# Kernel optimization log

Measured on AMD Instinct MI355X. Metric: run time of the kernel, lower is better.

Reference implementation:

```python
import jax, jax.numpy as jnp
import numpy as np

N = 50000   # nodes
E = 800000  # edges (avg degree 16)
H = 128     # hidden_dim / emb_dim
OUT = 128   # out_dim
NUM_BOND_TYPE = 6
NUM_BOND_DIR = 6


def setup_inputs() -> dict:
    key = jax.random.key(0)
    ks = jax.random.split(key, 12)
    s = 0.05
    return {
        "x": jax.random.normal(ks[0], (N, H), jnp.float32),
        "edge_index": jax.random.randint(ks[1], (2, E), 0, N),
        "edge_attr": jax.random.randint(ks[2], (E, 2), 0, 6),
        "prelu_a": jnp.float32(0.25),  # PReLU single shared slope (torch default)
        "W_enc": jax.random.normal(ks[3], (H, H), jnp.float32) * s,  # enc_to_dec, no bias
        "edge_emb1": jax.random.normal(ks[4], (NUM_BOND_TYPE, H), jnp.float32) * s,
        "edge_emb2": jax.random.normal(ks[5], (NUM_BOND_DIR, H), jnp.float32) * s,
        "W1": jax.random.normal(ks[6], (H, 2 * H), jnp.float32) * s,
        "b1": jnp.zeros((2 * H,), jnp.float32),
        "W2": jax.random.normal(ks[7], (2 * H, OUT), jnp.float32) * s,
        "b2": jnp.zeros((OUT,), jnp.float32),
    }


def reference(x, edge_index, edge_attr, prelu_a, W_enc, edge_emb1, edge_emb2, W1, b1, W2, b2):
    n = x.shape[0]
    # GNNDecoder: PReLU then enc_to_dec linear (no bias)
    x = jnp.where(x > 0, x, prelu_a * x)
    x = x @ W_enc

    # GINConv.forward: add self loops, self-loop edge_attr = [5, 0]
    loop = jnp.arange(n)
    src = jnp.concatenate([edge_index[0], loop])  # [E+N]
    dst = jnp.concatenate([edge_index[1], loop])  # [E+N]
    ea1 = jnp.concatenate([edge_attr[:, 0], jnp.full((n,), 5, edge_attr.dtype)])
    ea2 = jnp.concatenate([edge_attr[:, 1], jnp.zeros((n,), edge_attr.dtype)])

    # edge embedding lookup + gather-add message + scatter-add aggregate
    edge_emb = edge_emb1[ea1] + edge_emb2[ea2]          # [E+N, H]
    msg = x[src] + edge_emb                             # message(x_j, edge_attr)
    agg = jax.ops.segment_sum(msg, dst, num_segments=n)  # aggr='add'

    # update: MLP Linear(H,2H) -> SiLU -> Linear(2H,OUT)
    h = jax.nn.silu(agg @ W1 + b1)
    return h @ W2 + b2
```

## Files before the change

### kernel.cpp

```cpp
#include <hip/hip_runtime.h>

typedef unsigned short u16;
typedef unsigned int   u32;
typedef __attribute__((ext_vector_type(8))) short short8;
typedef __attribute__((ext_vector_type(4))) float f32x4;

__device__ __forceinline__ float bl(u32 u){ union{u32 i; float f;} c; c.i = u << 16; return c.f; }
__device__ __forceinline__ float bh(u32 u){ union{u32 i; float f;} c; c.i = u & 0xffff0000u; return c.f; }
__device__ __forceinline__ u16 f2b(float f){
  union{float f; u32 i;} c; c.f = f;
  return (u16)((c.i + 0x8000u) >> 16);
}
__device__ __forceinline__ u32 pk2(float a, float b){
  union{float f; u32 i;} x, y; x.f = a; y.f = b;
  return ((x.i + 0x8000u) >> 16) | ((y.i + 0x8000u) & 0xffff0000u);
}
__device__ __forceinline__ void acc4(float* a, uint2 xq, uint2 eq){
  a[0] += bl(xq.x) + bl(eq.x);  a[1] += bh(xq.x) + bh(eq.x);
  a[2] += bl(xq.y) + bl(eq.y);  a[3] += bh(xq.y) + bh(eq.y);
}

__global__ __launch_bounds__(256) void k_setup(
    const float* __restrict__ Wenc, const float* __restrict__ W1,
    const float* __restrict__ W2, u16* __restrict__ WencT,
    u16* __restrict__ W1T, u16* __restrict__ W2T,
    int* __restrict__ cnt, int N)
{
  int i = blockIdx.x * 256 + threadIdx.x;
  if (i < 16384) {
    int n = i >> 7, k = i & 127;
    WencT[i] = f2b(Wenc[k * 128 + n]);
  } else if (i < 49152) {
    int j = i - 16384;
    int n = j >> 7, k = j & 127;
    W1T[j] = f2b(W1[k * 256 + n]);
  } else if (i < 81920) {
    int j = i - 49152;
    int n = j >> 8, k = j & 255;
    W2T[j] = f2b(W2[k * 128 + n]);
  } else {
    int j = i - 81920;
    if (j < N) cnt[j] = 0;
  }
}

__global__ __launch_bounds__(256) void k_enc_count(
    const float* __restrict__ x, const float* __restrict__ pa,
    const u16* __restrict__ WT, u16* __restrict__ xenc, int N,
    const int* __restrict__ ei, int* __restrict__ cnt,
    int* __restrict__ rank, int E, int encBlocks)
{
  if ((int)blockIdx.x >= encBlocks) {
    int e = ((int)blockIdx.x - encBlocks) * 256 + threadIdx.x;
    if (e < E) rank[e] = atomicAdd(&cnt[ei[E + e]], 1);
    return;
  }

  const int K = 128, SK = 136, NT = 8;
  __shared__ u16 sB[128 * SK];

  const int t = threadIdx.x;
  #pragma unroll
  for (int j = 0; j < 8; j++) {
    int i = t + 256 * j;
    int n = i >> 4, k8 = i & 15;
    *(uint4*)&sB[n * SK + k8 * 8] = *(const uint4*)&WT[n * K + k8 * 8];
  }
  __syncthreads();

  const float slope = pa[0];
  const int lane = t & 63, wave = t >> 6, quad = lane >> 4, l16 = lane & 15;
  const int m0 = blockIdx.x * 128 + wave * 32;
  if (m0 >= N) return;

  f32x4 acc[2][NT];
  #pragma unroll
  for (int mr = 0; mr < 2; mr++)
    #pragma unroll
    for (int nt = 0; nt < NT; nt++) acc[mr][nt] = (f32x4){0.f, 0.f, 0.f, 0.f};

  #pragma unroll
  for (int ks = 0; ks < 4; ks++) {
    const int k0 = ks * 32 + quad * 8;
    union { u32 u[4]; short8 s; } a[2];
    #pragma unroll
    for (int mr = 0; mr < 2; mr++) {
      int row = m0 + mr * 16 + l16; row = min(row, N - 1);
      const float4* ap = (const float4*)&x[(size_t)row * 128 + k0];
      float4 f0 = ap[0], f1 = ap[1];
      float v0 = f0.x > 0.f ? f0.x : slope * f0.x;
      float v1 = f0.y > 0.f ? f0.y : slope * f0.y;
      float v2 = f0.z > 0.f ? f0.z : slope * f0.z;
      float v3 = f0.w > 0.f ? f0.w : slope * f0.w;
      float v4 = f1.x > 0.f ? f1.x : slope * f1.x;
      float v5 = f1.y > 0.f ? f1.y : slope * f1.y;
      float v6 = f1.z > 0.f ? f1.z : slope * f1.z;
      float v7 = f1.w > 0.f ? f1.w : slope * f1.w;
      a[mr].u[0] = pk2(v0, v1); a[mr].u[1] = pk2(v2, v3);
      a[mr].u[2] = pk2(v4, v5); a[mr].u[3] = pk2(v6, v7);
    }
    #pragma unroll
    for (int nt = 0; nt < NT; nt++) {
      short8 b = *(const short8*)&sB[(nt * 16 + l16) * SK + k0];
      acc[0][nt] = __builtin_amdgcn_mfma_f32_16x16x32_bf16(a[0].s, b, acc[0][nt], 0, 0, 0);
      acc[1][nt] = __builtin_amdgcn_mfma_f32_16x16x32_bf16(a[1].s, b, acc[1][nt], 0, 0, 0);
    }
  }

  #pragma unroll
  for (int mr = 0; mr < 2; mr++)
    #pragma unroll
    for (int nt = 0; nt < NT; nt++) {
      int col = nt * 16 + l16;
      #pragma unroll
      for (int r = 0; r < 4; r++) {
        int row = m0 + mr * 16 + quad * 4 + r;
        if (row < N) xenc[(size_t)row * 128 + col] = f2b(acc[mr][nt][r]);
      }
    }
}

__global__ __launch_bounds__(256) void k_scan_block(
    const int* __restrict__ cnt, int* __restrict__ offs,
    int* __restrict__ bsum, int n)
{
  __shared__ int sS[256];
  const int b = blockIdx.x, t = threadIdx.x;
  const int i0 = b * 1024 + t * 4;
  int4 v = make_int4(0, 0, 0, 0);
  if (i0 + 3 < n) v = *(const int4*)&cnt[i0];
  else {
    if (i0     < n) v.x = cnt[i0];
    if (i0 + 1 < n) v.y = cnt[i0 + 1];
    if (i0 + 2 < n) v.z = cnt[i0 + 2];
  }
  int s = v.x + v.y + v.z + v.w;
  sS[t] = s;
  __syncthreads();
  for (int d = 1; d < 256; d <<= 1) {
    int val = (t >= d) ? sS[t - d] : 0;
    __syncthreads();
    sS[t] += val;
    __syncthreads();
  }
  int ex = sS[t] - s;
  if (t == 255) bsum[b] = sS[t];
  int o0 = ex, o1 = o0 + v.x, o2 = o1 + v.y, o3 = o2 + v.z;
  if (i0     < n) offs[i0]     = o0;
  if (i0 + 1 < n) offs[i0 + 1] = o1;
  if (i0 + 2 < n) offs[i0 + 2] = o2;
  if (i0 + 3 < n) offs[i0 + 3] = o3;
}

__global__ __launch_bounds__(256) void k_scan_add(
    int* __restrict__ offs, const int* __restrict__ bsum,
    int nb, int n, int E)
{
  __shared__ int sOff;
  const int t = threadIdx.x;
  const int i = blockIdx.x * 256 + t;
  const int myb = (blockIdx.x * 256) >> 10;
  if (t == 0) {
    int s = 0;
    for (int j = 0; j < myb; j++) s += bsum[j];
    sOff = s;
  }
  __syncthreads();
  if (i < n) offs[i] += sOff;
  if (i == n) offs[n] = E;
}

__global__ __launch_bounds__(256) void k_fill(
    const int* __restrict__ ei, const int* __restrict__ ea,
    const int* __restrict__ offs, const int* __restrict__ rank,
    u32* __restrict__ recs, int E)
{
  int e = blockIdx.x * 256 + threadIdx.x;
  if (e >= E) return;
  int src = ei[e];
  int dst = ei[E + e];
  int2 a = *(const int2*)&ea[2 * e];
  int pos = offs[dst] + rank[e];
  recs[pos] = (u32)src | ((u32)(a.x * 6 + a.y) << 26);
}

__global__ __launch_bounds__(256) void k_gather(
    const int* __restrict__ offs, const u32* __restrict__ recs,
    const float* __restrict__ e1, const float* __restrict__ e2,
    const u32* __restrict__ xenc32, u32* __restrict__ aggb, int N)
{
  __shared__ u32 sE[36 * 64];

  const int t = threadIdx.x;
  for (int i = t; i < 36 * 64; i += 256) {
    int comb = i >> 6, l = i & 63;
    int c1 = comb / 6, c2 = comb - c1 * 6;
    float2 v1 = *(const float2*)&e1[c1 * 128 + 2 * l];
    float2 v2 = *(const float2*)&e2[c2 * 128 + 2 * l];
    sE[i] = pk2(v1.x + v2.x, v1.y + v2.y);
  }
  __syncthreads();

  const int v = blockIdx.x * 4 + (t >> 6);
  if (v >= N) return;
  const int lane = t & 63, g = lane >> 5, sub = lane & 31;
  const u32 M = 0x3ffffffu;

  float a[4];
  #pragma unroll
  for (int j = 0; j < 4; j++) a[j] = 0.f;

  if (g == 0) {
    uint2 xq = *(const uint2*)&xenc32[(size_t)v * 64 + sub * 2];
    uint2 eq = *(const uint2*)&sE[30 * 64 + sub * 2];
    acc4(a, xq, eq);
  }

  const int beg = offs[v], end = offs[v + 1];
  for (int base = beg; base < end; base += 64) {
    u32 rv = 0;
    if (base + lane < end) rv = recs[base + lane];
    const int cnt = min(64, end - base);
    const int npair = cnt >> 1;
    int jj = 0;
    for (; jj + 4 <= npair; jj += 4) {
      u32 r0 = __shfl(rv, (jj + 0) * 2 + g);
      u32 r1 = __shfl(rv, (jj + 1) * 2 + g);
      u32 r2 = __shfl(rv, (jj + 2) * 2 + g);
      u32 r3 = __shfl(rv, (jj + 3) * 2 + g);
      uint2 x0 = *(const uint2*)&xenc32[(size_t)(r0 & M) * 64 + sub * 2];
      uint2 x1 = *(const uint2*)&xenc32[(size_t)(r1 & M) * 64 + sub * 2];
      uint2 x2 = *(const uint2*)&xenc32[(size_t)(r2 & M) * 64 + sub * 2];
      uint2 x3 = *(const uint2*)&xenc32[(size_t)(r3 & M) * 64 + sub * 2];
      uint2 e0 = *(const uint2*)&sE[(r0 >> 26) * 64 + sub * 2];
      uint2 e1q = *(const uint2*)&sE[(r1 >> 26) * 64 + sub * 2];
      uint2 e2q = *(const uint2*)&sE[(r2 >> 26) * 64 + sub * 2];
      uint2 e3q = *(const uint2*)&sE[(r3 >> 26) * 64 + sub * 2];
      acc4(a, x0, e0); acc4(a, x1, e1q); acc4(a, x2, e2q); acc4(a, x3, e3q);
    }
    for (; jj < npair; jj++) {
      u32 r = __shfl(rv, jj * 2 + g);
      uint2 xq = *(const uint2*)&xenc32[(size_t)(r & M) * 64 + sub * 2];
      uint2 eq = *(const uint2*)&sE[(r >> 26) * 64 + sub * 2];
      acc4(a, xq, eq);
    }
    if (cnt & 1) {
      u32 r = __shfl(rv, cnt - 1);
      if (g == 0) {
        uint2 xq = *(const uint2*)&xenc32[(size_t)(r & M) * 64 + sub * 2];
        uint2 eq = *(const uint2*)&sE[(r >> 26) * 64 + sub * 2];
        acc4(a, xq, eq);
      }
    }
  }

  #pragma unroll
  for (int j = 0; j < 4; j++) a[j] += __shfl_xor(a[j], 32);

  if (g == 0) {
    uint2 o;
    o.x = pk2(a[0], a[1]);
    o.y = pk2(a[2], a[3]);
    *(uint2*)&aggb[(size_t)v * 64 + sub * 2] = o;
  }
}

__global__ __launch_bounds__(256) void k_mlp(
    const u16* __restrict__ aggb, const u16* __restrict__ W1T,
    const float* __restrict__ b1, const u16* __restrict__ W2T,
    const float* __restrict__ b2, float* __restrict__ out, int N)
{
  const int SK = 136;
  __shared__ u16 sW[128 * SK];
  __shared__ u16 sH[128 * SK];
  __shared__ float sB1[256];
  __shared__ float sB2[128];

  const int t = threadIdx.x;
  const int lane = t & 63, wave = t >> 6, quad = lane >> 4, l16 = lane & 15;
  const int m0 = blockIdx.x * 128 + wave * 32;

  if (t < 128) sB2[t] = b2[t];
  sB1[t] = b1[t];

  union { uint4 q; short8 s; } a[2][4];
  #pragma unroll
  for (int mr = 0; mr < 2; mr++) {
    int row = min(m0 + mr * 16 + l16, N - 1);
    #pragma unroll
    for (int ks = 0; ks < 4; ks++)
      a[mr][ks].q = *(const uint4*)&aggb[(size_t)row * 128 + ks * 32 + quad * 8];
  }

  f32x4 acc2[2][8];
  #pragma unroll
  for (int mr = 0; mr < 2; mr++)
    #pragma unroll
    for (int nt = 0; nt < 8; nt++) acc2[mr][nt] = (f32x4){0.f, 0.f, 0.f, 0.f};

  for (int half = 0; half < 2; half++) {
    #pragma unroll
    for (int j = 0; j < 8; j++) {
      int i = t + 256 * j;
      int n = i >> 4, k8 = i & 15;
      *(uint4*)&sW[n * SK + k8 * 8] =
          *(const uint4*)&W1T[(size_t)(half * 128 + n) * 128 + k8 * 8];
    }
    __syncthreads();

    f32x4 acc1[2][8];
    #pragma unroll
    for (int mr = 0; mr < 2; mr++)
      #pragma unroll
      for (int nt = 0; nt < 8; nt++) acc1[mr][nt] = (f32x4){0.f, 0.f, 0.f, 0.f};

    #pragma unroll
    for (int ks = 0; ks < 4; ks++) {
      const int k0 = ks * 32 + quad * 8;
      #pragma unroll
      for (int nt = 0; nt < 8; nt++) {
        short8 b = *(const short8*)&sW[(nt * 16 + l16) * SK + k0];
        acc1[0][nt] = __builtin_amdgcn_mfma_f32_16x16x32_bf16(a[0][ks].s, b, acc1[0][nt], 0, 0, 0);
        acc1[1][nt] = __builtin_amdgcn_mfma_f32_16x16x32_bf16(a[1][ks].s, b, acc1[1][nt], 0, 0, 0);
      }
    }

    #pragma unroll
    for (int mr = 0; mr < 2; mr++)
      #pragma unroll
      for (int nt = 0; nt < 8; nt++) {
        int col = nt * 16 + l16;
        float bias = sB1[half * 128 + col];
        #pragma unroll
        for (int r = 0; r < 4; r++) {
          float z = acc1[mr][nt][r] + bias;
          float s = z / (1.f + __expf(-z));
          sH[(wave * 32 + mr * 16 + quad * 4 + r) * SK + col] = f2b(s);
        }
      }
    __syncthreads();

    #pragma unroll
    for (int j = 0; j < 8; j++) {
      int i = t + 256 * j;
      int n = i >> 4, k8 = i & 15;
      *(uint4*)&sW[n * SK + k8 * 8] =
          *(const uint4*)&W2T[(size_t)n * 256 + half * 128 + k8 * 8];
    }
    __syncthreads();

    #pragma unroll
    for (int ks = 0; ks < 4; ks++) {
      const int k0 = ks * 32 + quad * 8;
      union { uint4 q; short8 s; } ah[2];
      #pragma unroll
      for (int mr = 0; mr < 2; mr++)
        ah[mr].q = *(const uint4*)&sH[(wave * 32 + mr * 16 + l16) * SK + k0];
      #pragma unroll
      for (int nt = 0; nt < 8; nt++) {
        short8 b = *(const short8*)&sW[(nt * 16 + l16) * SK + k0];
        acc2[0][nt] = __builtin_amdgcn_mfma_f32_16x16x32_bf16(ah[0].s, b, acc2[0][nt], 0, 0, 0);
        acc2[1][nt] = __builtin_amdgcn_mfma_f32_16x16x32_bf16(ah[1].s, b, acc2[1][nt], 0, 0, 0);
      }
    }
    __syncthreads();
  }

  #pragma unroll
  for (int mr = 0; mr < 2; mr++)
    #pragma unroll
    for (int nt = 0; nt < 8; nt++) {
      int col = nt * 16 + l16;
      float bias = sB2[col];
      #pragma unroll
      for (int r = 0; r < 4; r++) {
        int row = m0 + mr * 16 + quad * 4 + r;
        if (row < N) out[(size_t)row * 128 + col] = acc2[mr][nt][r] + bias;
      }
    }
}

extern "C" void kernel_launch(void* const* d_in, const int* in_sizes, int n_in,
                              void* d_out, int out_size, void* d_ws, size_t ws_size,
                              hipStream_t stream) {
  const float* x    = (const float*)d_in[0];
  const int*   ei   = (const int*)d_in[1];
  const int*   ea   = (const int*)d_in[2];
  const float* pa   = (const float*)d_in[3];
  const float* Wenc = (const float*)d_in[4];
  const float* e1   = (const float*)d_in[5];
  const float* e2   = (const float*)d_in[6];
  const float* W1   = (const float*)d_in[7];
  const float* b1   = (const float*)d_in[8];
  const float* W2   = (const float*)d_in[9];
  const float* b2   = (const float*)d_in[10];
  float* out = (float*)d_out;

  const int N = in_sizes[0] / 128;
  const int E = in_sizes[1] / 2;

  char* ws = (char*)d_ws;
  size_t off = 0;
  auto alloc = [&](size_t bytes) {
    void* p = ws + off;
    off = (off + bytes + 255) & ~(size_t)255;
    return p;
  };
  u16*   xenc   = (u16*)  alloc((size_t)N * 128 * 2);
  u32*   aggb   = (u32*)  alloc((size_t)N * 64 * 4);
  int*   cnt    = (int*)  alloc((size_t)N * 4);
  int*   offs   = (int*)  alloc((size_t)(N + 1) * 4);
  int*   rank   = (int*)  alloc((size_t)E * 4);
  int*   bsum   = (int*)  alloc(256 * 4);
  u32*   recs   = (u32*)  alloc((size_t)E * 4);
  u16*   WencT  = (u16*)  alloc(128 * 128 * 2);
  u16*   W1T    = (u16*)  alloc(256 * 128 * 2);
  u16*   W2T    = (u16*)  alloc(128 * 256 * 2);

  const int encBlocks   = (N + 127) / 128;
  const int edgeBlocks  = (E + 255) / 256;
  const int setupBlocks = (81920 + N + 255) / 256;
  const int nb          = (N + 1023) / 1024;

  k_setup<<<setupBlocks, 256, 0, stream>>>(Wenc, W1, W2, WencT, W1T, W2T, cnt, N);
  k_enc_count<<<encBlocks + edgeBlocks, 256, 0, stream>>>(
      x, pa, WencT, xenc, N, ei, cnt, rank, E, encBlocks);
  k_scan_block<<<nb, 256, 0, stream>>>(cnt, offs, bsum, N);
  k_scan_add<<<(N + 256) / 256, 256, 0, stream>>>(offs, bsum, nb, N, E);
  k_fill<<<edgeBlocks, 256, 0, stream>>>(ei, ea, offs, rank, recs, E);
  k_gather<<<(N + 3) / 4, 256, 0, stream>>>(
      offs, recs, e1, e2, (const u32*)xenc, aggb, N);
  k_mlp<<<encBlocks, 256, 0, stream>>>(
      (const u16*)aggb, W1T, b1, W2T, b2, out, N);
}
```

Before: 236.5 us.

## Drop scan-add kernel, fold block prefix into fill/gather; fp32 edge table; unroll 8

Result: no change. 237.8 us (+0.6%).

```diff
diff --git a/kernel.cpp b/kernel.cpp
--- a/kernel.cpp
+++ b/kernel.cpp
@@ -15,16 +15,35 @@
   union{float f; u32 i;} x, y; x.f = a; y.f = b;
   return ((x.i + 0x8000u) >> 16) | ((y.i + 0x8000u) & 0xffff0000u);
 }
-__device__ __forceinline__ void acc4(float* a, uint2 xq, uint2 eq){
-  a[0] += bl(xq.x) + bl(eq.x);  a[1] += bh(xq.x) + bh(eq.x);
-  a[2] += bl(xq.y) + bl(eq.y);  a[3] += bh(xq.y) + bh(eq.y);
+__device__ __forceinline__ void accf(float* a, uint2 xq, float4 ef){
+  a[0] += bl(xq.x) + ef.x;  a[1] += bh(xq.x) + ef.y;
+  a[2] += bl(xq.y) + ef.z;  a[3] += bh(xq.y) + ef.w;
+}
+
+__device__ __forceinline__ void wave_scan_bsum(
+    const int* __restrict__ bsum, int nb, int* __restrict__ sPre, int t)
+{
+  int carry = 0;
+  for (int c0 = 0; c0 < nb; c0 += 64) {
+    int idx = c0 + t;
+    int b = (idx < nb) ? bsum[idx] : 0;
+    int v = b;
+    #pragma unroll
+    for (int d = 1; d < 64; d <<= 1) {
+      int u = __shfl_up(v, d);
+      if (t >= d) v += u;
+    }
+    if (idx < nb) sPre[idx] = carry + v - b;
+    carry += __shfl(v, 63);
+  }
 }
 
 __global__ __launch_bounds__(256) void k_setup(
     const float* __restrict__ Wenc, const float* __restrict__ W1,
-    const float* __restrict__ W2, u16* __restrict__ WencT,
+    const float* __restrict__ W2, const float* __restrict__ e1,
+    const float* __restrict__ e2, u16* __restrict__ WencT,
     u16* __restrict__ W1T, u16* __restrict__ W2T,
-    int* __restrict__ cnt, int N)
+    float* __restrict__ embF, int* __restrict__ cnt, int N)
 {
   int i = blockIdx.x * 256 + threadIdx.x;
   if (i < 16384) {
@@ -38,8 +57,13 @@
     int j = i - 49152;
     int n = j >> 8, k = j & 255;
     W2T[j] = f2b(W2[k * 128 + n]);
+  } else if (i < 81920 + 4608) {
+    int j = i - 81920;
+    int comb = j >> 7, k = j & 127;
+    int c1 = comb / 6, c2 = comb - c1 * 6;
+    embF[j] = e1[c1 * 128 + k] + e2[c2 * 128 + k];
   } else {
-    int j = i - 81920;
+    int j = i - 81920 - 4608;
     if (j < N) cnt[j] = 0;
   }
 }
@@ -152,53 +176,38 @@
   if (i0 + 3 < n) offs[i0 + 3] = o3;
 }
 
-__global__ __launch_bounds__(256) void k_scan_add(
-    int* __restrict__ offs, const int* __restrict__ bsum,
-    int nb, int n, int E)
-{
-  __shared__ int sOff;
-  const int t = threadIdx.x;
-  const int i = blockIdx.x * 256 + t;
-  const int myb = (blockIdx.x * 256) >> 10;
-  if (t == 0) {
-    int s = 0;
-    for (int j = 0; j < myb; j++) s += bsum[j];
-    sOff = s;
-  }
-  __syncthreads();
-  if (i < n) offs[i] += sOff;
-  if (i == n) offs[n] = E;
-}
-
 __global__ __launch_bounds__(256) void k_fill(
     const int* __restrict__ ei, const int* __restrict__ ea,
     const int* __restrict__ offs, const int* __restrict__ rank,
+    const int* __restrict__ bsum, int nb,
     u32* __restrict__ recs, int E)
 {
-  int e = blockIdx.x * 256 + threadIdx.x;
+  __shared__ int sPre[256];
+  const int t = threadIdx.x;
+  if (t < 64) wave_scan_bsum(bsum, nb, sPre, t);
+  __syncthreads();
+
+  int e = blockIdx.x * 256 + t;
   if (e >= E) return;
   int src = ei[e];
   int dst = ei[E + e];
   int2 a = *(const int2*)&ea[2 * e];
-  int pos = offs[dst] + rank[e];
+  int pos = offs[dst] + sPre[dst >> 10] + rank[e];
   recs[pos] = (u32)src | ((u32)(a.x * 6 + a.y) << 26);
 }
 
 __global__ __launch_bounds__(256) void k_gather(
-    const int* __restrict__ offs, const u32* __restrict__ recs,
-    const float* __restrict__ e1, const float* __restrict__ e2,
-    const u32* __restrict__ xenc32, u32* __restrict__ aggb, int N)
-{
-  __shared__ u32 sE[36 * 64];
+    const int* __restrict__ offs, const int* __restrict__ bsum, int nb,
+    const u32* __restrict__ recs, const float* __restrict__ embF,
+    const u32* __restrict__ xenc32, u32* __restrict__ aggb, int N, int E)
+{
+  __shared__ float sE[36 * 128];
+  __shared__ int sPre[256];
 
   const int t = threadIdx.x;
-  for (int i = t; i < 36 * 64; i += 256) {
-    int comb = i >> 6, l = i & 63;
-    int c1 = comb / 6, c2 = comb - c1 * 6;
-    float2 v1 = *(const float2*)&e1[c1 * 128 + 2 * l];
-    float2 v2 = *(const float2*)&e2[c2 * 128 + 2 * l];
-    sE[i] = pk2(v1.x + v2.x, v1.y + v2.y);
-  }
+  for (int i = t; i < 1152; i += 256)
+    ((float4*)sE)[i] = ((const float4*)embF)[i];
+  if (t < 64) wave_scan_bsum(bsum, nb, sPre, t);
   __syncthreads();
 
   const int v = blockIdx.x * 4 + (t >> 6);
@@ -212,44 +221,59 @@
 
   if (g == 0) {
     uint2 xq = *(const uint2*)&xenc32[(size_t)v * 64 + sub * 2];
-    uint2 eq = *(const uint2*)&sE[30 * 64 + sub * 2];
-    acc4(a, xq, eq);
-  }
-
-  const int beg = offs[v], end = offs[v + 1];
+    float4 eq = *(const float4*)&sE[30 * 128 + sub * 4];
+    accf(a, xq, eq);
+  }
+
+  const int beg = offs[v] + sPre[v >> 10];
+  const int end = (v == N - 1) ? E : (offs[v + 1] + sPre[(v + 1) >> 10]);
+
   for (int base = beg; base < end; base += 64) {
     u32 rv = 0;
     if (base + lane < end) rv = recs[base + lane];
     const int cnt = min(64, end - base);
     const int npair = cnt >> 1;
     int jj = 0;
-    for (; jj + 4 <= npair; jj += 4) {
+    for (; jj + 8 <= npair; jj += 8) {
       u32 r0 = __shfl(rv, (jj + 0) * 2 + g);
       u32 r1 = __shfl(rv, (jj + 1) * 2 + g);
       u32 r2 = __shfl(rv, (jj + 2) * 2 + g);
       u32 r3 = __shfl(rv, (jj + 3) * 2 + g);
+      u32 r4 = __shfl(rv, (jj + 4) * 2 + g);
+      u32 r5 = __shfl(rv, (jj + 5) * 2 + g);
+      u32 r6 = __shfl(rv, (jj + 6) * 2 + g);
+      u32 r7 = __shfl(rv, (jj + 7) * 2 + g);
       uint2 x0 = *(const uint2*)&xenc32[(size_t)(r0 & M) * 64 + sub * 2];
       uint2 x1 = *(const uint2*)&xenc32[(size_t)(r1 & M) * 64 + sub * 2];
       uint2 x2 = *(const uint2*)&xenc32[(size_t)(r2 & M) * 64 + sub * 2];
       uint2 x3 = *(const uint2*)&xenc32[(size_t)(r3 & M) * 64 + sub * 2];
-      uint2 e0 = *(const uint2*)&sE[(r0 >> 26) * 64 + sub * 2];
-      uint2 e1q = *(const uint2*)&sE[(r1 >> 26) * 64 + sub * 2];
-      uint2 e2q = *(const uint2*)&sE[(r2 >> 26) * 64 + sub * 2];
-      uint2 e3q = *(const uint2*)&sE[(r3 >> 26) * 64 + sub * 2];
-      acc4(a, x0, e0); acc4(a, x1, e1q); acc4(a, x2, e2q); acc4(a, x3, e3q);
+      uint2 x4 = *(const uint2*)&xenc32[(size_t)(r4 & M) * 64 + sub * 2];
+      uint2 x5 = *(const uint2*)&xenc32[(size_t)(r5 & M) * 64 + sub * 2];
+      uint2 x6 = *(const uint2*)&xenc32[(size_t)(r6 & M) * 64 + sub * 2];
+      uint2 x7 = *(const uint2*)&xenc32[(size_t)(r7 & M) * 64 + sub * 2];
+      float4 e0 = *(const float4*)&sE[(r0 >> 26) * 128 + sub * 4];
+      float4 e1 = *(const float4*)&sE[(r1 >> 26) * 128 + sub * 4];
+      float4 e2 = *(const float4*)&sE[(r2 >> 26) * 128 + sub * 4];
+      float4 e3 = *(const float4*)&sE[(r3 >> 26) * 128 + sub * 4];
+      float4 e4 = *(const float4*)&sE[(r4 >> 26) * 128 + sub * 4];
+      float4 e5 = *(const float4*)&sE[(r5 >> 26) * 128 + sub * 4];
+      float4 e6 = *(const float4*)&sE[(r6 >> 26) * 128 + sub * 4];
+      float4 e7 = *(const float4*)&sE[(r7 >> 26) * 128 + sub * 4];
+      accf(a, x0, e0); accf(a, x1, e1); accf(a, x2, e2); accf(a, x3, e3);
+      accf(a, x4, e4); accf(a, x5, e5); accf(a, x6, e6); accf(a, x7, e7);
     }
     for (; jj < npair; jj++) {
       u32 r = __shfl(rv, jj * 2 + g);
       uint2 xq = *(const uint2*)&xenc32[(size_t)(r & M) * 64 + sub * 2];
-      uint2 eq = *(const uint2*)&sE[(r >> 26) * 64 + sub * 2];
-      acc4(a, xq, eq);
+      float4 eq = *(const float4*)&sE[(r >> 26) * 128 + sub * 4];
+      accf(a, xq, eq);
     }
     if (cnt & 1) {
       u32 r = __shfl(rv, cnt - 1);
       if (g == 0) {
         uint2 xq = *(const uint2*)&xenc32[(size_t)(r & M) * 64 + sub * 2];
-        uint2 eq = *(const uint2*)&sE[(r >> 26) * 64 + sub * 2];
-        acc4(a, xq, eq);
+        float4 eq = *(const float4*)&sE[(r >> 26) * 128 + sub * 4];
+        accf(a, xq, eq);
       }
     }
   }
@@ -416,20 +440,21 @@
   u16*   WencT  = (u16*)  alloc(128 * 128 * 2);
   u16*   W1T    = (u16*)  alloc(256 * 128 * 2);
   u16*   W2T    = (u16*)  alloc(128 * 256 * 2);
+  float* embF   = (float*)alloc(36 * 128 * 4);
 
   const int encBlocks   = (N + 127) / 128;
   const int edgeBlocks  = (E + 255) / 256;
-  const int setupBlocks = (81920 + N + 255) / 256;
+  const int setupBlocks = (81920 + 4608 + N + 255) / 256;
   const int nb          = (N + 1023) / 1024;
 
-  k_setup<<<setupBlocks, 256, 0, stream>>>(Wenc, W1, W2, WencT, W1T, W2T, cnt, N);
+  k_setup<<<setupBlocks, 256, 0, stream>>>(Wenc, W1, W2, e1, e2,
+                                           WencT, W1T, W2T, embF, cnt, N);
   k_enc_count<<<encBlocks + edgeBlocks, 256, 0, stream>>>(
       x, pa, WencT, xenc, N, ei, cnt, rank, E, encBlocks);
   k_scan_block<<<nb, 256, 0, stream>>>(cnt, offs, bsum, N);
-  k_scan_add<<<(N + 256) / 256, 256, 0, stream>>>(offs, bsum, nb, N, E);
-  k_fill<<<edgeBlocks, 256, 0, stream>>>(ei, ea, offs, rank, recs, E);
+  k_fill<<<edgeBlocks, 256, 0, stream>>>(ei, ea, offs, rank, bsum, nb, recs, E);
   k_gather<<<(N + 3) / 4, 256, 0, stream>>>(
-      offs, recs, e1, e2, (const u32*)xenc, aggb, N);
+      offs, bsum, nb, recs, embF, (const u32*)xenc, aggb, N, E);
   k_mlp<<<encBlocks, 256, 0, stream>>>(
       (const u16*)aggb, W1T, b1, W2T, b2, out, N);
 }
```
